# Kernel optimization log

Hardware: AMD Instinct MI355X
Metric: run time of the kernel (lower is better)

Reference implementation:

```python
import jax, jax.numpy as jnp
import numpy as np
from jax import lax

DIVISOR = 2.0
POOL = 2

def setup_inputs() -> dict:
    key = jax.random.key(0)
    k1, k2, k3, k4 = jax.random.split(key, 4)
    x = jax.random.normal(k1, (16, 8, 16, 128, 128), dtype=jnp.float32)
    conv_weight = jax.random.normal(k2, (32, 8, 3, 3, 3), dtype=jnp.float32) * 0.05
    conv_bias = jax.random.normal(k3, (32,), dtype=jnp.float32) * 0.05
    bias = jax.random.normal(k4, (32, 1, 1, 1), dtype=jnp.float32)
    return {"x": x, "conv_weight": conv_weight, "conv_bias": conv_bias, "bias": bias}

def reference(x, conv_weight, conv_bias, bias):
    # Conv3d, valid padding, stride 1: [B,Cin,D,H,W] -> [B,Cout,D-2,H-2,W-2]
    y = lax.conv_general_dilated(
        x, conv_weight,
        window_strides=(1, 1, 1), padding="VALID",
        dimension_numbers=("NCDHW", "OIDHW", "NCDHW"))
    y = y + conv_bias[None, :, None, None, None]
    y = y / DIVISOR
    # MaxPool3d(2): non-overlapping 2x2x2 windows, floor mode
    y = lax.reduce_window(
        y, -jnp.inf, lax.max,
        window_dimensions=(1, 1, POOL, POOL, POOL),
        window_strides=(1, 1, POOL, POOL, POOL),
        padding="VALID")
    # AdaptiveAvgPool3d((1,1,1)) -> [B,C,1,1,1]
    y = jnp.mean(y, axis=(2, 3, 4), keepdims=True)
    # bias add (C,1,1,1) then sum over channel dim (sum_dim=1)
    y = y + bias
    return jnp.sum(y, axis=1)  # [B,1,1,1]
```

## Files before the change

### kernel.cpp

```cpp
#include <hip/hip_runtime.h>
#include <math.h>

namespace {

constexpr int B = 16, CIN = 8, D = 16, H = 128, W = 128;
constexpr int COUT = 32;
constexpr int PD = 7, PH = 63, PW = 63;
constexpr float INV_CNT = 1.0f / (float)(PD * PH * PW);
constexpr int DHW = D * H * W;

typedef short v8s __attribute__((ext_vector_type(8)));
typedef float v16f __attribute__((ext_vector_type(16)));

constexpr int WB_OFF = 32768, RED_OFF = 47104, LDS_BYTES = RED_OFF + 64;

__device__ inline unsigned short f2bf(float f) {
    unsigned int x = __builtin_bit_cast(unsigned int, f);
    return (unsigned short)((x + 0x7FFFu + ((x >> 16) & 1u)) >> 16);
}

__global__ void init_out_kernel(const float* __restrict__ bias, float* __restrict__ out) {
    int b = threadIdx.x;
    if (b < B) {
        float s = 0.f;
        #pragma unroll
        for (int c = 0; c < COUT; ++c) s += bias[c];
        out[b] = s;
    }
}

__global__ __launch_bounds__(512, 2) void conv_mfma_kernel(
    const float* __restrict__ x,
    const float* __restrict__ wgt,
    const float* __restrict__ cbias,
    float* __restrict__ out)
{
    __shared__ __align__(16) char smem[LDS_BYTES];

    const int bid = blockIdx.x;
    const int logical = (bid & 7) * 882 + (bid >> 3);
    const int ph = logical % 63;
    const int pd = (logical / 63) % 7;
    const int b  = logical / 441;

    const int t    = threadIdx.x;
    const int lane = t & 63;
    const int wv   = t >> 6;

    for (int pr = t; pr < 14 * 64; pr += 512) {
        const int p = pr >> 6, l = pr & 63;
        const int tap = 2 * p + (l >> 5);
        const int cout = l & 31;
        uint4 pk = {0u, 0u, 0u, 0u};
        if (tap < 27) {
            unsigned int v[4];
            #pragma unroll
            for (int j = 0; j < 4; ++j) {
                unsigned short b0 = f2bf(wgt[(cout * CIN + 2 * j) * 27 + tap]);
                unsigned short b1 = f2bf(wgt[(cout * CIN + 2 * j + 1) * 27 + tap]);
                v[j] = (unsigned int)b0 | ((unsigned int)b1 << 16);
            }
            pk.x = v[0]; pk.y = v[1]; pk.z = v[2]; pk.w = v[3];
        }
        *reinterpret_cast<uint4*>(smem + WB_OFF + pr * 16) = pk;
    }

    const float* xb = x + (size_t)b * CIN * DHW;
    for (int s = t; s < 2048; s += 512) {
        const int d = s >> 9, h = (s >> 7) & 3, w = s & 127;
        const float* xp = xb + (2 * pd + d) * (H * W) + (2 * ph + h) * W + w;
        unsigned int v[4];
        #pragma unroll
        for (int j = 0; j < 4; ++j) {
            unsigned short b0 = f2bf(xp[(2 * j) * DHW]);
            unsigned short b1 = f2bf(xp[(2 * j + 1) * DHW]);
            v[j] = (unsigned int)b0 | ((unsigned int)b1 << 16);
        }
        const int byte = (((d * 4 + h) * 128 + w) * 16) ^ ((h & 1) << 6);
        *reinterpret_cast<uint4*>(smem + byte) = uint4{v[0], v[1], v[2], v[3]};
    }

    __syncthreads();

    const int r    = lane & 31;
    const int half = lane >> 5;
    const int hh   = r >> 4;
    const int pwl  = (r >> 1) & 7;
    const int ww   = r & 1;
    const int wbase = 2 * (8 * wv + pwl) + ww;

    v16f acc0, acc1;
    #pragma unroll
    for (int i = 0; i < 16; ++i) { acc0[i] = 0.f; acc1[i] = 0.f; }

    #pragma unroll
    for (int ks = 0; ks < 14; ++ks) {
        const int t0 = 2 * ks, t1 = t0 + 1;
        const int KD0 = t0 / 9, KH0 = (t0 % 9) / 3, KW0 = t0 % 3;
        const int KD1 = (t1 < 27) ? t1 / 9 : 0;
        const int KH1 = (t1 < 27) ? (t1 % 9) / 3 : 0;
        const int KW1 = (t1 < 27) ? t1 % 3 : 0;
        const int kd = half ? KD1 : KD0;
        const int kh = half ? KH1 : KH0;
        const int kw = half ? KW1 : KW0;
        const int h = hh + kh;
        int w = wbase + kw; w = (w > 127) ? 127 : w;
        const int byte = (((kd * 4 + h) * 128 + w) * 16) ^ ((h & 1) << 6);

        const v8s A0 = *reinterpret_cast<const v8s*>(smem + byte);
        const v8s A1 = *reinterpret_cast<const v8s*>(smem + byte + 8192);
        const v8s Bf = *reinterpret_cast<const v8s*>(smem + WB_OFF + (ks * 64 + lane) * 16);
        acc0 = __builtin_amdgcn_mfma_f32_32x32x16_bf16(A0, Bf, acc0, 0, 0, 0);
        acc1 = __builtin_amdgcn_mfma_f32_32x32x16_bf16(A1, Bf, acc1, 0, 0, 0);
    }

    const float cb = cbias[lane & 31];
    float lsum = 0.f;
    #pragma unroll
    for (int j = 0; j < 4; ++j) {
        float m = fmaxf(fmaxf(acc0[2 * j], acc0[2 * j + 1]),
                        fmaxf(acc0[8 + 2 * j], acc0[9 + 2 * j]));
        m = fmaxf(m, fmaxf(fmaxf(acc1[2 * j], acc1[2 * j + 1]),
                           fmaxf(acc1[8 + 2 * j], acc1[9 + 2 * j])));
        const int pw = 8 * wv + ((j & 1) + ((j >> 1) << 2) + 2 * half);
        if (pw < PW) lsum += (m + cb) * 0.5f;
    }

    #pragma unroll
    for (int o = 32; o > 0; o >>= 1) lsum += __shfl_xor(lsum, o, 64);
    if (lane == 0) *reinterpret_cast<float*>(smem + RED_OFF + wv * 4) = lsum;
    __syncthreads();
    if (t == 0) {
        float s = 0.f;
        #pragma unroll
        for (int i = 0; i < 8; ++i) s += reinterpret_cast<float*>(smem + RED_OFF)[i];
        atomicAdd(&out[b], s * INV_CNT);
    }
}

}

extern "C" void kernel_launch(void* const* d_in, const int* in_sizes, int n_in,
                              void* d_out, int out_size, void* d_ws, size_t ws_size,
                              hipStream_t stream) {
    const float* x     = (const float*)d_in[0];
    const float* wgt   = (const float*)d_in[1];
    const float* cbias = (const float*)d_in[2];
    const float* bias  = (const float*)d_in[3];
    float* out = (float*)d_out;

    hipLaunchKernelGGL(init_out_kernel, dim3(1), dim3(64), 0, stream, bias, out);
    hipLaunchKernelGGL(conv_mfma_kernel, dim3(B * PD * PH), dim3(512), 0, stream,
                       x, wgt, cbias, out);
}
```

Baseline: 287.2 us.

## Stage full depth per block and loop pooled depth to reuse input slices

Each block now covers one (batch, pooled-row) pair and stages all 16 depth slices of its four input rows in LDS (about 128 KB). It then loops over the 7 pooled depths, so overlapping depth halos are no longer reloaded from global memory. Weight fragments and A-operand offsets are hoisted into registers for reuse across the depth loop. The atomicAdd accumulation is replaced by per-block partials and a small finalize kernel. The cost is a much larger LDS footprint, which likely allows only one block per CU, plus fewer blocks and less overlap between loading and MFMA work.

Result: faster. 242.9 us (-15.4%).

```diff
diff --git a/kernel.cpp b/kernel.cpp
--- a/kernel.cpp
+++ b/kernel.cpp
@@ -4,53 +4,40 @@
 namespace {
 
 constexpr int B = 16, CIN = 8, D = 16, H = 128, W = 128;
-constexpr int COUT = 32;
-constexpr int PD = 7, PH = 63, PW = 63;
-constexpr float INV_CNT = 1.0f / (float)(PD * PH * PW);
-constexpr int DHW = D * H * W;
+constexpr int PW = 63;
+constexpr float INV_CNT = 1.0f / 27783.0f;
+constexpr int HW = H * W, DHW = D * HW;
 
-typedef short v8s __attribute__((ext_vector_type(8)));
+typedef short v8s  __attribute__((ext_vector_type(8)));
 typedef float v16f __attribute__((ext_vector_type(16)));
 
-constexpr int WB_OFF = 32768, RED_OFF = 47104, LDS_BYTES = RED_OFF + 64;
+constexpr int WB_OFF = 131072;
+constexpr int RED_OFF = WB_OFF + 14336;
+constexpr int LDS_BYTES = RED_OFF + 64;
 
 __device__ inline unsigned short f2bf(float f) {
     unsigned int x = __builtin_bit_cast(unsigned int, f);
     return (unsigned short)((x + 0x7FFFu + ((x >> 16) & 1u)) >> 16);
 }
 
-__global__ void init_out_kernel(const float* __restrict__ bias, float* __restrict__ out) {
-    int b = threadIdx.x;
-    if (b < B) {
-        float s = 0.f;
-        #pragma unroll
-        for (int c = 0; c < COUT; ++c) s += bias[c];
-        out[b] = s;
-    }
-}
-
 __global__ __launch_bounds__(512, 2) void conv_mfma_kernel(
     const float* __restrict__ x,
     const float* __restrict__ wgt,
     const float* __restrict__ cbias,
-    float* __restrict__ out)
+    float* __restrict__ partials)
 {
     __shared__ __align__(16) char smem[LDS_BYTES];
 
     const int bid = blockIdx.x;
-    const int logical = (bid & 7) * 882 + (bid >> 3);
+    const int logical = (bid & 7) * 126 + (bid >> 3);
     const int ph = logical % 63;
-    const int pd = (logical / 63) % 7;
-    const int b  = logical / 441;
+    const int b  = logical / 63;
 
-    const int t    = threadIdx.x;
-    const int lane = t & 63;
-    const int wv   = t >> 6;
+    const int t = threadIdx.x, lane = t & 63, wv = t >> 6;
 
     for (int pr = t; pr < 14 * 64; pr += 512) {
         const int p = pr >> 6, l = pr & 63;
-        const int tap = 2 * p + (l >> 5);
-        const int cout = l & 31;
+        const int tap = 2 * p + (l >> 5), cout = l & 31;
         uint4 pk = {0u, 0u, 0u, 0u};
         if (tap < 27) {
             unsigned int v[4];
@@ -60,15 +47,16 @@
                 unsigned short b1 = f2bf(wgt[(cout * CIN + 2 * j + 1) * 27 + tap]);
                 v[j] = (unsigned int)b0 | ((unsigned int)b1 << 16);
             }
-            pk.x = v[0]; pk.y = v[1]; pk.z = v[2]; pk.w = v[3];
+            pk = uint4{v[0], v[1], v[2], v[3]};
         }
         *reinterpret_cast<uint4*>(smem + WB_OFF + pr * 16) = pk;
     }
 
     const float* xb = x + (size_t)b * CIN * DHW;
-    for (int s = t; s < 2048; s += 512) {
+    #pragma unroll 4
+    for (int s = t; s < 8192; s += 512) {
         const int d = s >> 9, h = (s >> 7) & 3, w = s & 127;
-        const float* xp = xb + (2 * pd + d) * (H * W) + (2 * ph + h) * W + w;
+        const float* xp = xb + d * HW + (2 * ph + h) * W + w;
         unsigned int v[4];
         #pragma unroll
         for (int j = 0; j < 4; ++j) {
@@ -76,23 +64,22 @@
             unsigned short b1 = f2bf(xp[(2 * j + 1) * DHW]);
             v[j] = (unsigned int)b0 | ((unsigned int)b1 << 16);
         }
-        const int byte = (((d * 4 + h) * 128 + w) * 16) ^ ((h & 1) << 6);
+        const int byte = (s * 16) ^ ((h & 1) << 6);
         *reinterpret_cast<uint4*>(smem + byte) = uint4{v[0], v[1], v[2], v[3]};
     }
 
     __syncthreads();
 
-    const int r    = lane & 31;
-    const int half = lane >> 5;
-    const int hh   = r >> 4;
-    const int pwl  = (r >> 1) & 7;
-    const int ww   = r & 1;
+    v8s Bf[14];
+    #pragma unroll
+    for (int ks = 0; ks < 14; ++ks)
+        Bf[ks] = *reinterpret_cast<const v8s*>(smem + WB_OFF + (ks * 64 + lane) * 16);
+
+    const int r = lane & 31, half = lane >> 5;
+    const int hh = r >> 4, pwl = (r >> 1) & 7, ww = r & 1;
     const int wbase = 2 * (8 * wv + pwl) + ww;
 
-    v16f acc0, acc1;
-    #pragma unroll
-    for (int i = 0; i < 16; ++i) { acc0[i] = 0.f; acc1[i] = 0.f; }
-
+    int offA[14];
     #pragma unroll
     for (int ks = 0; ks < 14; ++ks) {
         const int t0 = 2 * ks, t1 = t0 + 1;
@@ -105,25 +92,36 @@
         const int kw = half ? KW1 : KW0;
         const int h = hh + kh;
         int w = wbase + kw; w = (w > 127) ? 127 : w;
-        const int byte = (((kd * 4 + h) * 128 + w) * 16) ^ ((h & 1) << 6);
-
-        const v8s A0 = *reinterpret_cast<const v8s*>(smem + byte);
-        const v8s A1 = *reinterpret_cast<const v8s*>(smem + byte + 8192);
-        const v8s Bf = *reinterpret_cast<const v8s*>(smem + WB_OFF + (ks * 64 + lane) * 16);
-        acc0 = __builtin_amdgcn_mfma_f32_32x32x16_bf16(A0, Bf, acc0, 0, 0, 0);
-        acc1 = __builtin_amdgcn_mfma_f32_32x32x16_bf16(A1, Bf, acc1, 0, 0, 0);
+        offA[ks] = (((kd * 4 + h) * 128 + w) * 16) ^ ((h & 1) << 6);
     }
 
     const float cb = cbias[lane & 31];
     float lsum = 0.f;
-    #pragma unroll
-    for (int j = 0; j < 4; ++j) {
-        float m = fmaxf(fmaxf(acc0[2 * j], acc0[2 * j + 1]),
-                        fmaxf(acc0[8 + 2 * j], acc0[9 + 2 * j]));
-        m = fmaxf(m, fmaxf(fmaxf(acc1[2 * j], acc1[2 * j + 1]),
-                           fmaxf(acc1[8 + 2 * j], acc1[9 + 2 * j])));
-        const int pw = 8 * wv + ((j & 1) + ((j >> 1) << 2) + 2 * half);
-        if (pw < PW) lsum += (m + cb) * 0.5f;
+
+    #pragma unroll 1
+    for (int pd = 0; pd < 7; ++pd) {
+        v16f acc0, acc1;
+        #pragma unroll
+        for (int i = 0; i < 16; ++i) { acc0[i] = 0.f; acc1[i] = 0.f; }
+        const int pbase = pd * 16384;
+
+        #pragma unroll
+        for (int ks = 0; ks < 14; ++ks) {
+            const v8s A0 = *reinterpret_cast<const v8s*>(smem + pbase + offA[ks]);
+            const v8s A1 = *reinterpret_cast<const v8s*>(smem + pbase + offA[ks] + 8192);
+            acc0 = __builtin_amdgcn_mfma_f32_32x32x16_bf16(A0, Bf[ks], acc0, 0, 0, 0);
+            acc1 = __builtin_amdgcn_mfma_f32_32x32x16_bf16(A1, Bf[ks], acc1, 0, 0, 0);
+        }
+
+        #pragma unroll
+        for (int j = 0; j < 4; ++j) {
+            float m = fmaxf(fmaxf(acc0[2 * j], acc0[2 * j + 1]),
+                            fmaxf(acc0[8 + 2 * j], acc0[9 + 2 * j]));
+            m = fmaxf(m, fmaxf(fmaxf(acc1[2 * j], acc1[2 * j + 1]),
+                               fmaxf(acc1[8 + 2 * j], acc1[9 + 2 * j])));
+            const int pw = 8 * wv + ((j & 1) + ((j >> 1) << 2) + 2 * half);
+            if (pw < PW) lsum += (m + cb) * 0.5f;
+        }
     }
 
     #pragma unroll
@@ -134,8 +132,22 @@
         float s = 0.f;
         #pragma unroll
         for (int i = 0; i < 8; ++i) s += reinterpret_cast<float*>(smem + RED_OFF)[i];
-        atomicAdd(&out[b], s * INV_CNT);
+        partials[logical] = s;
     }
+}
+
+__global__ void finalize_kernel(const float* __restrict__ partials,
+                                const float* __restrict__ bias,
+                                float* __restrict__ out)
+{
+    const int t = threadIdx.x;
+    const int b = t >> 5, l = t & 31;
+    float s = 0.f;
+    for (int j = l; j < 63; j += 32) s += partials[b * 63 + j];
+    s = s * INV_CNT + bias[l];
+    #pragma unroll
+    for (int o = 16; o > 0; o >>= 1) s += __shfl_xor(s, o, 32);
+    if (l == 0) out[b] = s;
 }
 
 }
@@ -147,9 +159,11 @@
     const float* wgt   = (const float*)d_in[1];
     const float* cbias = (const float*)d_in[2];
     const float* bias  = (const float*)d_in[3];
-    float* out = (float*)d_out;
+    float* out      = (float*)d_out;
+    float* partials = (float*)d_ws;
 
-    hipLaunchKernelGGL(init_out_kernel, dim3(1), dim3(64), 0, stream, bias, out);
-    hipLaunchKernelGGL(conv_mfma_kernel, dim3(B * PD * PH), dim3(512), 0, stream,
-                       x, wgt, cbias, out);
+    hipLaunchKernelGGL(conv_mfma_kernel, dim3(B * 63), dim3(512), 0, stream,
+                       x, wgt, cbias, partials);
+    hipLaunchKernelGGL(finalize_kernel, dim3(1), dim3(512), 0, stream,
+                       partials, bias, out);
 }
```
